# Kernel optimization log

Hardware: AMD Instinct MI355X
Metric: run time of the kernel (lower is better)

Reference implementation:

```python
import jax, jax.numpy as jnp
import numpy as np
from itertools import permutations, product

K = 64
RADIUS = 0.15


def generate_24_rotations():
    # All signed permutation matrices with det=+1: the 24 rotations of the cube.
    mats = []
    for perm in permutations(range(3)):
        for signs in product([1.0, -1.0], repeat=3):
            M = np.zeros((3, 3), dtype=np.float32)
            for r in range(3):
                M[r, perm[r]] = signs[r]
            if np.linalg.det(M) > 0:
                mats.append(M)
    return jnp.asarray(np.stack(mats))  # [24, 3, 3]


def ball_group(x, y, k, radius):
    # x: [B, N, 3] queries, y: [B, M, 3] support points.
    # Returns relative coords of k neighbors within radius: [B, N, k, 3].
    d2 = jnp.sum((x[:, :, None, :] - y[:, None, :, :]) ** 2, axis=-1)  # [B,N,M]
    masked = jnp.where(d2 <= radius * radius, -d2, -jnp.inf)
    vals, idx = jax.lax.top_k(masked, k)                 # k nearest within ball
    nearest = jnp.argmin(d2, axis=-1)                    # fallback: global nearest
    idx = jnp.where(vals > -jnp.inf, idx, nearest[:, :, None])  # [B,N,k]
    gathered = jnp.take_along_axis(y[:, None, :, :],
                                   idx[:, :, :, None], axis=2)  # [B,N,k,3]
    return gathered - x[:, :, None, :]


def setup_inputs() -> dict:
    key = jax.random.key(0)
    kx, k1, k2, k3, k4 = jax.random.split(key, 5)
    B, N = 2, 1024
    x = jax.random.uniform(kx, (B, N, 3), dtype=jnp.float32)  # unit cube
    W1 = jax.random.normal(k1, (32, 3), dtype=jnp.float32) * 0.1
    b1 = jax.random.normal(k2, (32,), dtype=jnp.float32) * 0.1
    W2 = jax.random.normal(k3, (64, 32), dtype=jnp.float32) * 0.1
    b2 = jax.random.normal(k4, (64,), dtype=jnp.float32) * 0.1
    return {"x": x, "W1": W1, "b1": b1, "W2": W2, "b2": b2}


def reference(x, W1, b1, W2, b2):
    Rs = generate_24_rotations()  # [24,3,3]
    gp = ball_group(x, x, K, RADIUS)  # [B,N,K,3]
    # Faithful to torch.einsum('bnkj,ijj->bnikj', ...): repeated j takes the
    # DIAGONAL of each rotation matrix: out = gp[...,j] * Rs[i,j,j].
    gp = jnp.einsum('bnkj,ijj->bnikj', gp, Rs)       # [B,N,24,K,3]
    gp = jnp.transpose(gp, (0, 4, 1, 2, 3))          # [B,3,N,24,K]
    # 1x1x1 Conv3d == pointwise linear over channel dim, then ReLU.
    h = jax.nn.relu(jnp.einsum('bcnik,oc->bonik', gp, W1)
                    + b1[None, :, None, None, None])  # [B,32,N,24,K]
    h = jax.nn.relu(jnp.einsum('bcnik,oc->bonik', h, W2)
                    + b2[None, :, None, None, None])  # [B,64,N,24,K]
    f = jnp.max(h, axis=-1)   # max over neighbors  -> [B,64,N,24]
    f = jnp.mean(f, axis=-1)  # mean over rotations -> [B,64,N]
    return f
```

## Files before the change

kernel.cpp:

```cpp
#include <hip/hip_runtime.h>
#include <math.h>

typedef _Float16 half8 __attribute__((ext_vector_type(8)));
typedef float    f32x4 __attribute__((ext_vector_type(4)));

#define NPTS 1024
#define KMAX 64
#define R2   0.0225f

__global__ __launch_bounds__(256, 2) void point_encoder_kernel(
    const float* __restrict__ xg,
    const float* __restrict__ W1g,
    const float* __restrict__ b1g,
    const float* __restrict__ W2g,
    const float* __restrict__ b2g,
    float* __restrict__ outg)
{
    __shared__ float nbs[4][KMAX * 3];
    __shared__ float ost[4][64];

    const int tid  = threadIdx.x;
    const int wid  = tid >> 6;
    const int lane = tid & 63;
    const int kl   = lane & 15;
    const int quad = lane >> 4;

    const int p = blockIdx.x * 4 + wid;
    const int b = p >> 10;
    const int n = p & (NPTS - 1);

    float w1x[8], w1y[8], w1z[8], b1r[8];
    #pragma unroll
    for (int j = 0; j < 8; ++j) {
        const int c = quad * 8 + j;
        w1x[j] = W1g[c*3+0];
        w1y[j] = W1g[c*3+1];
        w1z[j] = W1g[c*3+2];
        b1r[j] = b1g[c];
    }
    half8 Bf[4];
    float b2v[4];
    #pragma unroll
    for (int nt = 0; nt < 4; ++nt) {
        const int o = nt * 16 + kl;
        #pragma unroll
        for (int j = 0; j < 8; ++j)
            Bf[nt][j] = (_Float16)W2g[o * 32 + quad * 8 + j];
        b2v[nt] = b2g[o];
    }

    float* nb = nbs[wid];
    nb[lane] = 0.f; nb[lane + 64] = 0.f; nb[lane + 128] = 0.f;
    const float* xb = xg + b * NPTS * 3;
    const float qx = xb[n*3+0], qy = xb[n*3+1], qz = xb[n*3+2];
    int base = 0;
    for (int it = 0; it < 16; ++it) {
        const int idx = it * 64 + lane;
        const float dx = xb[idx*3+0] - qx;
        const float dy = xb[idx*3+1] - qy;
        const float dz = xb[idx*3+2] - qz;
        const float d2 = dx*dx + dy*dy + dz*dz;
        const bool pred = (d2 <= R2);
        const unsigned long long mask = __ballot(pred);
        const int pos = base + __popcll(mask & ((1ull << lane) - 1ull));
        if (pred && pos < KMAX) {
            nb[pos*3+0] = dx; nb[pos*3+1] = dy; nb[pos*3+2] = dz;
        }
        base += __popcll(mask);
    }
    int cn = base < KMAX ? base : KMAX;
    const int ntiles = (cn + 15) >> 4;

    float mv[11][4];
    #pragma unroll
    for (int i = 0; i < 11; ++i)
        #pragma unroll
        for (int nt = 0; nt < 4; ++nt) mv[i][nt] = -INFINITY;

    for (int mt = 0; mt < ntiles; ++mt) {
        const int k = mt * 16 + kl;
        const float gx = nb[k*3+0], gy = nb[k*3+1], gz = nb[k*3+2];
        half8 A[11];
        #pragma unroll
        for (int j = 0; j < 8; ++j) {
            const float tx = w1x[j] * gx;
            const float ty = w1y[j] * gy;
            const float tz = w1z[j] * gz;
            const float pxy = tx + ty, mxy = tx - ty;
            const float bpz = b1r[j] + tz, bmz = b1r[j] - tz;
            A[0][j] = (_Float16)fmaxf(bpz + pxy, 0.f);
            A[1][j] = (_Float16)fmaxf(bmz + mxy, 0.f);
            A[2][j] = (_Float16)fmaxf(bmz - mxy, 0.f);
            A[3][j] = (_Float16)fmaxf(bpz - pxy, 0.f);
            A[4][j] = (_Float16)fmaxf(b1r[j] + tx, 0.f);
            A[5][j] = (_Float16)fmaxf(b1r[j] - tx, 0.f);
            A[6][j] = (_Float16)fmaxf(b1r[j] + ty, 0.f);
            A[7][j] = (_Float16)fmaxf(b1r[j] - ty, 0.f);
            A[8][j] = (_Float16)fmaxf(bpz, 0.f);
            A[9][j] = (_Float16)fmaxf(bmz, 0.f);
            A[10][j] = (_Float16)fmaxf(b1r[j], 0.f);
        }
        #pragma unroll
        for (int i = 0; i < 11; ++i) {
            if (i == 10 && mt != 0) continue;
            #pragma unroll
            for (int nt = 0; nt < 4; ++nt) {
                f32x4 C = {0.f, 0.f, 0.f, 0.f};
                C = __builtin_amdgcn_mfma_f32_16x16x32_f16(A[i], Bf[nt], C, 0, 0, 0);
                const float r = fmaxf(fmaxf(C[0], C[1]), fmaxf(C[2], C[3]));
                mv[i][nt] = fmaxf(mv[i][nt], r);
            }
        }
    }

    float acc[4] = {0.f, 0.f, 0.f, 0.f};
    #pragma unroll
    for (int i = 0; i < 11; ++i) {
        const float wgt = (i < 4) ? 1.f : (i < 10) ? 2.f : 8.f;
        #pragma unroll
        for (int nt = 0; nt < 4; ++nt) {
            float r = mv[i][nt];
            r = fmaxf(r, __shfl_xor(r, 16));
            r = fmaxf(r, __shfl_xor(r, 32));
            acc[nt] += wgt * fmaxf(r + b2v[nt], 0.f);
        }
    }

    const float f = (quad == 0 ? acc[0] : quad == 1 ? acc[1]
                   : quad == 2 ? acc[2] : acc[3]) * (1.f / 24.f);
    ost[wid][lane] = f;
    __syncthreads();
    if (tid < 64) {
        float4 v = make_float4(ost[0][tid], ost[1][tid], ost[2][tid], ost[3][tid]);
        const int n0 = (blockIdx.x * 4) & (NPTS - 1);
        const int bb = (blockIdx.x * 4) >> 10;
        *(float4*)(outg + (size_t)(bb * 64 + tid) * NPTS + n0) = v;
    }
}

extern "C" void kernel_launch(void* const* d_in, const int* in_sizes, int n_in,
                              void* d_out, int out_size, void* d_ws, size_t ws_size,
                              hipStream_t stream) {
    const float* x  = (const float*)d_in[0];
    const float* W1 = (const float*)d_in[1];
    const float* b1 = (const float*)d_in[2];
    const float* W2 = (const float*)d_in[3];
    const float* b2 = (const float*)d_in[4];
    float* out = (float*)d_out;

    const int total  = in_sizes[0] / 3;
    const int blocks = (total + 3) / 4;
    point_encoder_kernel<<<blocks, 256, 0, stream>>>(x, W1, b1, W2, b2, out);
}
```

Measured before the change: 80.91 us.

## Split each query point across four waves by rotation class

Switches from one wave per query point to one 256-thread block per point. The four waves scan disjoint quarters of the point cloud and append neighbours into a shared list through an atomic counter. Each wave then handles a subset of the 11 distinct rotation classes, with the constant bias-only class done once, and the weighted partial sums are reduced in shared memory. W1, W2 and b2 are staged once per block in LDS, and launch bounds are raised to allow more blocks per CU. The goal is to cut per-wave serial MFMA work and register pressure, at the cost of 4x more blocks, extra block-wide syncs, unbalanced per-wave work, and scalar rather than vectorised output stores. The atomic append also makes neighbour order nondeterministic, though the max over neighbours is unaffected.

```diff
diff --git a/kernel.cpp b/kernel.cpp
--- a/kernel.cpp
+++ b/kernel.cpp
@@ -8,7 +8,7 @@
 #define KMAX 64
 #define R2   0.0225f
 
-__global__ __launch_bounds__(256, 2) void point_encoder_kernel(
+__global__ __launch_bounds__(256, 4) void point_encoder_kernel(
     const float* __restrict__ xg,
     const float* __restrict__ W1g,
     const float* __restrict__ b1g,
@@ -16,8 +16,12 @@
     const float* __restrict__ b2g,
     float* __restrict__ outg)
 {
-    __shared__ float nbs[4][KMAX * 3];
+    __shared__ __align__(16) float    w1b[32 * 4];
+    __shared__ __align__(16) _Float16 W2h[64 * 32];
+    __shared__ float b2s[64];
+    __shared__ float nb[KMAX * 3];
     __shared__ float ost[4][64];
+    __shared__ int   cnt;
 
     const int tid  = threadIdx.x;
     const int wid  = tid >> 6;
@@ -25,116 +29,136 @@
     const int kl   = lane & 15;
     const int quad = lane >> 4;
 
-    const int p = blockIdx.x * 4 + wid;
-    const int b = p >> 10;
-    const int n = p & (NPTS - 1);
+    const int b = blockIdx.x >> 10;
+    const int n = blockIdx.x & (NPTS - 1);
 
-    float w1x[8], w1y[8], w1z[8], b1r[8];
+    if (tid < 32) {
+        w1b[tid*4+0] = W1g[tid*3+0];
+        w1b[tid*4+1] = W1g[tid*3+1];
+        w1b[tid*4+2] = W1g[tid*3+2];
+        w1b[tid*4+3] = b1g[tid];
+    }
     #pragma unroll
-    for (int j = 0; j < 8; ++j) {
-        const int c = quad * 8 + j;
-        w1x[j] = W1g[c*3+0];
-        w1y[j] = W1g[c*3+1];
-        w1z[j] = W1g[c*3+2];
-        b1r[j] = b1g[c];
-    }
+    for (int i = 0; i < 8; ++i) W2h[i*256 + tid] = (_Float16)W2g[i*256 + tid];
+    if (tid < 64)       b2s[tid] = b2g[tid];
+    if (tid < KMAX * 3) nb[tid]  = 0.f;
+    if (tid == 0)       cnt = 0;
+    __syncthreads();
+
+    f32x4 w1r[8];
+    #pragma unroll
+    for (int j = 0; j < 8; ++j)
+        w1r[j] = *(const f32x4*)&w1b[(quad*8 + j) * 4];
     half8 Bf[4];
     float b2v[4];
     #pragma unroll
     for (int nt = 0; nt < 4; ++nt) {
-        const int o = nt * 16 + kl;
-        #pragma unroll
-        for (int j = 0; j < 8; ++j)
-            Bf[nt][j] = (_Float16)W2g[o * 32 + quad * 8 + j];
-        b2v[nt] = b2g[o];
+        Bf[nt]  = *(const half8*)&W2h[(nt*16 + kl) * 32 + quad * 8];
+        b2v[nt] = b2s[nt*16 + kl];
     }
 
-    float* nb = nbs[wid];
-    nb[lane] = 0.f; nb[lane + 64] = 0.f; nb[lane + 128] = 0.f;
     const float* xb = xg + b * NPTS * 3;
     const float qx = xb[n*3+0], qy = xb[n*3+1], qz = xb[n*3+2];
-    int base = 0;
-    for (int it = 0; it < 16; ++it) {
-        const int idx = it * 64 + lane;
+    #pragma unroll
+    for (int it = 0; it < 4; ++it) {
+        const int idx = wid * 256 + it * 64 + lane;
         const float dx = xb[idx*3+0] - qx;
         const float dy = xb[idx*3+1] - qy;
         const float dz = xb[idx*3+2] - qz;
         const float d2 = dx*dx + dy*dy + dz*dz;
         const bool pred = (d2 <= R2);
         const unsigned long long mask = __ballot(pred);
-        const int pos = base + __popcll(mask & ((1ull << lane) - 1ull));
+        const int cit = __popcll(mask);
+        int base0 = 0;
+        if (lane == 0 && cit) base0 = atomicAdd(&cnt, cit);
+        base0 = __shfl(base0, 0, 64);
+        const int pos = base0 + __popcll(mask & ((1ull << lane) - 1ull));
         if (pred && pos < KMAX) {
             nb[pos*3+0] = dx; nb[pos*3+1] = dy; nb[pos*3+2] = dz;
         }
-        base += __popcll(mask);
     }
-    int cn = base < KMAX ? base : KMAX;
+    __syncthreads();
+    int cn = cnt; if (cn > KMAX) cn = KMAX;
     const int ntiles = (cn + 15) >> 4;
 
-    float mv[11][4];
+    float mvc[4] = {0.f, 0.f, 0.f, 0.f};
+    if (wid == 3) {
+        half8 Ac;
+        #pragma unroll
+        for (int j = 0; j < 8; ++j) Ac[j] = (_Float16)fmaxf(w1r[j].w, 0.f);
+        #pragma unroll
+        for (int nt = 0; nt < 4; ++nt) {
+            f32x4 C = {0.f, 0.f, 0.f, 0.f};
+            C = __builtin_amdgcn_mfma_f32_16x16x32_f16(Ac, Bf[nt], C, 0, 0, 0);
+            mvc[nt] = fmaxf(fmaxf(C[0], C[1]), fmaxf(C[2], C[3]));
+        }
+    }
+
+    const int nd = (wid < 2) ? 3 : 2;
+    float mv[3][4];
     #pragma unroll
-    for (int i = 0; i < 11; ++i)
+    for (int d = 0; d < 3; ++d)
         #pragma unroll
-        for (int nt = 0; nt < 4; ++nt) mv[i][nt] = -INFINITY;
+        for (int nt = 0; nt < 4; ++nt) mv[d][nt] = -INFINITY;
 
     for (int mt = 0; mt < ntiles; ++mt) {
         const int k = mt * 16 + kl;
         const float gx = nb[k*3+0], gy = nb[k*3+1], gz = nb[k*3+2];
-        half8 A[11];
+        half8 A[3];
         #pragma unroll
         for (int j = 0; j < 8; ++j) {
-            const float tx = w1x[j] * gx;
-            const float ty = w1y[j] * gy;
-            const float tz = w1z[j] * gz;
-            const float pxy = tx + ty, mxy = tx - ty;
-            const float bpz = b1r[j] + tz, bmz = b1r[j] - tz;
-            A[0][j] = (_Float16)fmaxf(bpz + pxy, 0.f);
-            A[1][j] = (_Float16)fmaxf(bmz + mxy, 0.f);
-            A[2][j] = (_Float16)fmaxf(bmz - mxy, 0.f);
-            A[3][j] = (_Float16)fmaxf(bpz - pxy, 0.f);
-            A[4][j] = (_Float16)fmaxf(b1r[j] + tx, 0.f);
-            A[5][j] = (_Float16)fmaxf(b1r[j] - tx, 0.f);
-            A[6][j] = (_Float16)fmaxf(b1r[j] + ty, 0.f);
-            A[7][j] = (_Float16)fmaxf(b1r[j] - ty, 0.f);
-            A[8][j] = (_Float16)fmaxf(bpz, 0.f);
-            A[9][j] = (_Float16)fmaxf(bmz, 0.f);
-            A[10][j] = (_Float16)fmaxf(b1r[j], 0.f);
+            const float tx = w1r[j].x * gx;
+            const float ty = w1r[j].y * gy;
+            const float tz = w1r[j].z * gz;
+            const float bb = w1r[j].w;
+            float a0, a1, a2 = 0.f;
+            if (wid == 0)      { a0 = bb+tx+ty+tz; a1 = bb+tx-ty-tz; a2 = bb-tx+ty-tz; }
+            else if (wid == 1) { a0 = bb-tx-ty+tz; a1 = bb+tx;       a2 = bb-tx;       }
+            else if (wid == 2) { a0 = bb+ty;       a1 = bb-ty;                          }
+            else               { a0 = bb+tz;       a1 = bb-tz;                          }
+            A[0][j] = (_Float16)fmaxf(a0, 0.f);
+            A[1][j] = (_Float16)fmaxf(a1, 0.f);
+            A[2][j] = (_Float16)fmaxf(a2, 0.f);
         }
         #pragma unroll
-        for (int i = 0; i < 11; ++i) {
-            if (i == 10 && mt != 0) continue;
+        for (int d = 0; d < 3; ++d) {
+            if (d >= nd) break;
             #pragma unroll
             for (int nt = 0; nt < 4; ++nt) {
                 f32x4 C = {0.f, 0.f, 0.f, 0.f};
-                C = __builtin_amdgcn_mfma_f32_16x16x32_f16(A[i], Bf[nt], C, 0, 0, 0);
+                C = __builtin_amdgcn_mfma_f32_16x16x32_f16(A[d], Bf[nt], C, 0, 0, 0);
                 const float r = fmaxf(fmaxf(C[0], C[1]), fmaxf(C[2], C[3]));
-                mv[i][nt] = fmaxf(mv[i][nt], r);
+                mv[d][nt] = fmaxf(mv[d][nt], r);
             }
         }
     }
 
-    float acc[4] = {0.f, 0.f, 0.f, 0.f};
+    float accv[4] = {0.f, 0.f, 0.f, 0.f};
     #pragma unroll
-    for (int i = 0; i < 11; ++i) {
-        const float wgt = (i < 4) ? 1.f : (i < 10) ? 2.f : 8.f;
+    for (int d = 0; d < 3; ++d) {
+        if (d >= nd) break;
+        const float wgt = (wid == 0 || (wid == 1 && d == 0)) ? 1.f : 2.f;
         #pragma unroll
         for (int nt = 0; nt < 4; ++nt) {
-            float r = mv[i][nt];
-            r = fmaxf(r, __shfl_xor(r, 16));
-            r = fmaxf(r, __shfl_xor(r, 32));
-            acc[nt] += wgt * fmaxf(r + b2v[nt], 0.f);
+            float r = mv[d][nt];
+            r = fmaxf(r, __shfl_xor(r, 16, 64));
+            r = fmaxf(r, __shfl_xor(r, 32, 64));
+            accv[nt] += wgt * fmaxf(r + b2v[nt], 0.f);
         }
     }
+    if (wid == 3) {
+        #pragma unroll
+        for (int nt = 0; nt < 4; ++nt)
+            accv[nt] += 8.f * fmaxf(mvc[nt] + b2v[nt], 0.f);
+    }
 
-    const float f = (quad == 0 ? acc[0] : quad == 1 ? acc[1]
-                   : quad == 2 ? acc[2] : acc[3]) * (1.f / 24.f);
-    ost[wid][lane] = f;
+    ost[wid][lane] = (quad == 0) ? accv[0] : (quad == 1) ? accv[1]
+                   : (quad == 2) ? accv[2] : accv[3];
     __syncthreads();
     if (tid < 64) {
-        float4 v = make_float4(ost[0][tid], ost[1][tid], ost[2][tid], ost[3][tid]);
-        const int n0 = (blockIdx.x * 4) & (NPTS - 1);
-        const int bb = (blockIdx.x * 4) >> 10;
-        *(float4*)(outg + (size_t)(bb * 64 + tid) * NPTS + n0) = v;
+        const float s = (ost[0][tid] + ost[1][tid] + ost[2][tid] + ost[3][tid])
+                        * (1.f / 24.f);
+        outg[(size_t)b * (64 * NPTS) + (size_t)tid * NPTS + n] = s;
     }
 }
 
@@ -148,7 +172,6 @@
     const float* b2 = (const float*)d_in[4];
     float* out = (float*)d_out;
 
-    const int total  = in_sizes[0] / 3;
-    const int blocks = (total + 3) / 4;
-    point_encoder_kernel<<<blocks, 256, 0, stream>>>(x, W1, b1, W2, b2, out);
+    const int total = in_sizes[0] / 3;
+    point_encoder_kernel<<<total, 256, 0, stream>>>(x, W1, b1, W2, b2, out);
 }
```

Measured after the change: 75.72 us. 1.07x faster.

## Assign one point per block and split channels and neighbor scan across waves

Applied to the files above, without the earlier changes.

Each block now handles a single query point instead of four. The four waves each take one 16-wide output-channel tile and a quarter of the neighbor scan, compacting neighbors into shared memory with a per-wave atomicAdd. This cuts per-wave registers (10 running maxima instead of 44, one B fragment instead of four), raises launch bounds to 4 blocks per SIMD, and shortens each wave's serial scan. The costs are four times more blocks, two block barriers per point, an atomic on shared memory, and scalar output stores in place of float4 writes. Neighbor order becomes nondeterministic, which does not change the max.

```diff
diff --git a/kernel.cpp b/kernel.cpp
--- a/kernel.cpp
+++ b/kernel.cpp
@@ -8,7 +8,7 @@
 #define KMAX 64
 #define R2   0.0225f
 
-__global__ __launch_bounds__(256, 2) void point_encoder_kernel(
+__global__ __launch_bounds__(256, 4) void point_encoder_kernel(
     const float* __restrict__ xg,
     const float* __restrict__ W1g,
     const float* __restrict__ b1g,
@@ -16,71 +16,87 @@
     const float* __restrict__ b2g,
     float* __restrict__ outg)
 {
-    __shared__ float nbs[4][KMAX * 3];
-    __shared__ float ost[4][64];
+    __shared__ float nb[KMAX * 3];
+    __shared__ int   cnt;
 
     const int tid  = threadIdx.x;
-    const int wid  = tid >> 6;
+    const int nt   = tid >> 6;
     const int lane = tid & 63;
     const int kl   = lane & 15;
     const int quad = lane >> 4;
 
-    const int p = blockIdx.x * 4 + wid;
-    const int b = p >> 10;
-    const int n = p & (NPTS - 1);
+    const int b = blockIdx.x >> 10;
+    const int n = blockIdx.x & (NPTS - 1);
 
-    float w1x[8], w1y[8], w1z[8], b1r[8];
+    const int o = nt * 16 + kl;
+    const f32x4 w2a = *(const f32x4*)(W2g + o * 32 + quad * 8);
+    const f32x4 w2b = *(const f32x4*)(W2g + o * 32 + quad * 8 + 4);
+    const float b2v = b2g[o];
+    f32x4 w1raw[6];
     #pragma unroll
-    for (int j = 0; j < 8; ++j) {
-        const int c = quad * 8 + j;
-        w1x[j] = W1g[c*3+0];
-        w1y[j] = W1g[c*3+1];
-        w1z[j] = W1g[c*3+2];
-        b1r[j] = b1g[c];
-    }
-    half8 Bf[4];
-    float b2v[4];
-    #pragma unroll
-    for (int nt = 0; nt < 4; ++nt) {
-        const int o = nt * 16 + kl;
-        #pragma unroll
-        for (int j = 0; j < 8; ++j)
-            Bf[nt][j] = (_Float16)W2g[o * 32 + quad * 8 + j];
-        b2v[nt] = b2g[o];
-    }
+    for (int j = 0; j < 6; ++j)
+        w1raw[j] = *(const f32x4*)(W1g + quad * 24 + j * 4);
+    const f32x4 b1a = *(const f32x4*)(b1g + quad * 8);
+    const f32x4 b1b = *(const f32x4*)(b1g + quad * 8 + 4);
 
-    float* nb = nbs[wid];
-    nb[lane] = 0.f; nb[lane + 64] = 0.f; nb[lane + 128] = 0.f;
+    if (tid < KMAX * 3) nb[tid] = 0.f;
+    if (tid == 0)       cnt = 0;
+    __syncthreads();
+
     const float* xb = xg + b * NPTS * 3;
     const float qx = xb[n*3+0], qy = xb[n*3+1], qz = xb[n*3+2];
-    int base = 0;
-    for (int it = 0; it < 16; ++it) {
-        const int idx = it * 64 + lane;
+    #pragma unroll
+    for (int it = 0; it < 4; ++it) {
+        const int idx = nt * 256 + it * 64 + lane;
         const float dx = xb[idx*3+0] - qx;
         const float dy = xb[idx*3+1] - qy;
         const float dz = xb[idx*3+2] - qz;
         const float d2 = dx*dx + dy*dy + dz*dz;
         const bool pred = (d2 <= R2);
         const unsigned long long mask = __ballot(pred);
-        const int pos = base + __popcll(mask & ((1ull << lane) - 1ull));
+        const int cit = __popcll(mask);
+        int base0 = 0;
+        if (lane == 0 && cit) base0 = atomicAdd(&cnt, cit);
+        base0 = __shfl(base0, 0, 64);
+        const int pos = base0 + __popcll(mask & ((1ull << lane) - 1ull));
         if (pred && pos < KMAX) {
             nb[pos*3+0] = dx; nb[pos*3+1] = dy; nb[pos*3+2] = dz;
         }
-        base += __popcll(mask);
     }
-    int cn = base < KMAX ? base : KMAX;
+    __syncthreads();
+    int cn = cnt; if (cn > KMAX) cn = KMAX;
     const int ntiles = (cn + 15) >> 4;
 
-    float mv[11][4];
+    half8 Bf;
     #pragma unroll
-    for (int i = 0; i < 11; ++i)
-        #pragma unroll
-        for (int nt = 0; nt < 4; ++nt) mv[i][nt] = -INFINITY;
+    for (int j = 0; j < 4; ++j) {
+        Bf[j]     = (_Float16)w2a[j];
+        Bf[j + 4] = (_Float16)w2b[j];
+    }
+    float w1x[8], w1y[8], w1z[8], b1r[8];
+    #pragma unroll
+    for (int j = 0; j < 8; ++j) {
+        w1x[j] = w1raw[(j*3    ) >> 2][(j*3    ) & 3];
+        w1y[j] = w1raw[(j*3 + 1) >> 2][(j*3 + 1) & 3];
+        w1z[j] = w1raw[(j*3 + 2) >> 2][(j*3 + 2) & 3];
+        b1r[j] = (j < 4) ? b1a[j] : b1b[j - 4];
+    }
+
+    half8 Ac;
+    #pragma unroll
+    for (int j = 0; j < 8; ++j) Ac[j] = (_Float16)fmaxf(b1r[j], 0.f);
+    f32x4 Cc = {0.f, 0.f, 0.f, 0.f};
+    Cc = __builtin_amdgcn_mfma_f32_16x16x32_f16(Ac, Bf, Cc, 0, 0, 0);
+    float acc = 8.f * fmaxf(Cc[0] + b2v, 0.f);
+
+    float mv[10];
+    #pragma unroll
+    for (int i = 0; i < 10; ++i) mv[i] = -INFINITY;
 
     for (int mt = 0; mt < ntiles; ++mt) {
         const int k = mt * 16 + kl;
         const float gx = nb[k*3+0], gy = nb[k*3+1], gz = nb[k*3+2];
-        half8 A[11];
+        half8 A[10];
         #pragma unroll
         for (int j = 0; j < 8; ++j) {
             const float tx = w1x[j] * gx;
@@ -98,44 +114,24 @@
             A[7][j] = (_Float16)fmaxf(b1r[j] - ty, 0.f);
             A[8][j] = (_Float16)fmaxf(bpz, 0.f);
             A[9][j] = (_Float16)fmaxf(bmz, 0.f);
-            A[10][j] = (_Float16)fmaxf(b1r[j], 0.f);
         }
         #pragma unroll
-        for (int i = 0; i < 11; ++i) {
-            if (i == 10 && mt != 0) continue;
-            #pragma unroll
-            for (int nt = 0; nt < 4; ++nt) {
-                f32x4 C = {0.f, 0.f, 0.f, 0.f};
-                C = __builtin_amdgcn_mfma_f32_16x16x32_f16(A[i], Bf[nt], C, 0, 0, 0);
-                const float r = fmaxf(fmaxf(C[0], C[1]), fmaxf(C[2], C[3]));
-                mv[i][nt] = fmaxf(mv[i][nt], r);
-            }
+        for (int i = 0; i < 10; ++i) {
+            f32x4 C = {0.f, 0.f, 0.f, 0.f};
+            C = __builtin_amdgcn_mfma_f32_16x16x32_f16(A[i], Bf, C, 0, 0, 0);
+            mv[i] = fmaxf(mv[i], fmaxf(fmaxf(C[0], C[1]), fmaxf(C[2], C[3])));
         }
     }
 
-    float acc[4] = {0.f, 0.f, 0.f, 0.f};
     #pragma unroll
-    for (int i = 0; i < 11; ++i) {
-        const float wgt = (i < 4) ? 1.f : (i < 10) ? 2.f : 8.f;
-        #pragma unroll
-        for (int nt = 0; nt < 4; ++nt) {
-            float r = mv[i][nt];
-            r = fmaxf(r, __shfl_xor(r, 16));
-            r = fmaxf(r, __shfl_xor(r, 32));
-            acc[nt] += wgt * fmaxf(r + b2v[nt], 0.f);
-        }
+    for (int i = 0; i < 10; ++i) {
+        float r = mv[i];
+        r = fmaxf(r, __shfl_xor(r, 16, 64));
+        r = fmaxf(r, __shfl_xor(r, 32, 64));
+        acc += ((i < 4) ? 1.f : 2.f) * fmaxf(r + b2v, 0.f);
     }
-
-    const float f = (quad == 0 ? acc[0] : quad == 1 ? acc[1]
-                   : quad == 2 ? acc[2] : acc[3]) * (1.f / 24.f);
-    ost[wid][lane] = f;
-    __syncthreads();
-    if (tid < 64) {
-        float4 v = make_float4(ost[0][tid], ost[1][tid], ost[2][tid], ost[3][tid]);
-        const int n0 = (blockIdx.x * 4) & (NPTS - 1);
-        const int bb = (blockIdx.x * 4) >> 10;
-        *(float4*)(outg + (size_t)(bb * 64 + tid) * NPTS + n0) = v;
-    }
+    if (quad == 0)
+        outg[(size_t)b * (64 * NPTS) + (size_t)o * NPTS + n] = acc * (1.f / 24.f);
 }
 
 extern "C" void kernel_launch(void* const* d_in, const int* in_sizes, int n_in,
@@ -148,7 +144,6 @@
     const float* b2 = (const float*)d_in[4];
     float* out = (float*)d_out;
 
-    const int total  = in_sizes[0] / 3;
-    const int blocks = (total + 3) / 4;
-    point_encoder_kernel<<<blocks, 256, 0, stream>>>(x, W1, b1, W2, b2, out);
+    const int total = in_sizes[0] / 3;
+    point_encoder_kernel<<<total, 256, 0, stream>>>(x, W1, b1, W2, b2, out);
 }
```

Measured after the change: 75.26 us. -7.0%, faster.
